# Performance work log

Hardware: AMD Instinct MI355X
Metric: run time of the kernel (lower is better)

Reference implementation:

```python
import jax, jax.numpy as jnp
import numpy as np

N_NODES = 100000
N_EDGES = 1600000
IN_F, HID_F, OUT_F = 256, 128, 32


def spmm(rows, cols, vals, x):
    # out[i] = sum_{e: rows[e]==i} vals[e] * x[cols[e]]  -- COO SpMM
    msgs = vals[:, None] * x[cols]            # [E, F] gathered weighted messages
    return jax.ops.segment_sum(msgs, rows, num_segments=N_NODES)


def setup_inputs() -> dict:
    key = jax.random.key(0)
    k = jax.random.split(key, 6)
    x = jax.random.normal(k[0], (N_NODES, IN_F), dtype=jnp.float32)
    adj_rows = jax.random.randint(k[1], (N_EDGES,), 0, N_NODES, dtype=jnp.int32)
    adj_cols = jax.random.randint(k[2], (N_EDGES,), 0, N_NODES, dtype=jnp.int32)
    adj_vals = jax.random.uniform(k[3], (N_EDGES,), dtype=jnp.float32)
    W1 = jax.random.normal(k[4], (IN_F, HID_F), dtype=jnp.float32) / np.sqrt(IN_F)
    W2 = jax.random.normal(k[5], (HID_F, OUT_F), dtype=jnp.float32) / np.sqrt(HID_F)
    return {"x": x, "adj_rows": adj_rows, "adj_cols": adj_cols,
            "adj_vals": adj_vals, "W1": W1, "W2": W2}


def reference(x, adj_rows, adj_cols, adj_vals, W1, W2):
    # TwoLayerGCN forward (eval mode: dropout = identity, labels=None)
    h = spmm(adj_rows, adj_cols, adj_vals, x @ W1)   # conv1: linear then A_hat @
    h = jax.nn.relu(h)
    out = spmm(adj_rows, adj_cols, adj_vals, h @ W2)  # conv2
    return out
```

## Files before the change

### kernel.cpp

```cpp
#include <hip/hip_runtime.h>
#include <hip/hip_bf16.h>

#define N_NODES 100000
#define IN_F 256
#define HID_F 128
#define OUT_F 32
#define NBUCK 391
#define BCAP  5120
#define ACHUNK 4096
#define NCHUNKS ((1600000 + ACHUNK - 1) / ACHUNK)

typedef __bf16 bf16x8 __attribute__((ext_vector_type(8)));
typedef __bf16 bf16x2 __attribute__((ext_vector_type(2)));
typedef float  f32x4  __attribute__((ext_vector_type(4)));

__global__ void cvt_w1t_kernel(const float* __restrict__ W1, __bf16* __restrict__ W1T) {
    int i = blockIdx.x * 256 + threadIdx.x;
    if (i >= IN_F * HID_F) return;
    int n = i >> 8, k = i & 255;
    W1T[i] = (__bf16)W1[k * HID_F + n];
}

__device__ __forceinline__
void bucketize_body(char* smem, int blk,
                    const int* __restrict__ rows, const int* __restrict__ cols,
                    const float* __restrict__ vals, int* __restrict__ gcnt,
                    int2* __restrict__ staged, int E) {
    int2* lcv  = (int2*)smem;
    int* lcnt  = (int*)(smem + ACHUNK * 8);
    int* loff  = lcnt + NBUCK;
    int* lcur  = loff + NBUCK;
    int* gbase = lcur + NBUCK;
    int* psum  = gbase + NBUCK;

    const int t    = threadIdx.x;
    const int base = blk * ACHUNK;

    for (int b = t; b < NBUCK; b += 256) lcnt[b] = 0;
    __syncthreads();

    int myrow[16];
#pragma unroll
    for (int i = 0; i < 16; ++i) {
        int e = base + t + i * 256;
        int r = (e < E) ? rows[e] : -1;
        myrow[i] = r;
        if (r >= 0) atomicAdd(&lcnt[r >> 8], 1);
    }
    __syncthreads();

    int s0 = (t * 2     < NBUCK) ? lcnt[t * 2]     : 0;
    int s1 = (t * 2 + 1 < NBUCK) ? lcnt[t * 2 + 1] : 0;
    int local = s0 + s1;
    psum[t] = local;
    __syncthreads();
    for (int off = 1; off < 256; off <<= 1) {
        int v = (t >= off) ? psum[t - off] : 0;
        __syncthreads();
        psum[t] += v;
        __syncthreads();
    }
    int excl = psum[t] - local;
    if (t * 2     < NBUCK) { loff[t * 2]     = excl;      lcur[t * 2]     = excl; }
    if (t * 2 + 1 < NBUCK) { loff[t * 2 + 1] = excl + s0; lcur[t * 2 + 1] = excl + s0; }
    __syncthreads();

#pragma unroll
    for (int i = 0; i < 16; ++i) {
        int r = myrow[i];
        if (r >= 0) {
            int e = base + t + i * 256;
            int posl = atomicAdd(&lcur[r >> 8], 1);
            lcv[posl] = make_int2(cols[e] | ((r & 255) << 20), __float_as_int(vals[e]));
        }
    }
    __syncthreads();

    for (int b = t; b < NBUCK; b += 256) {
        int c = lcnt[b];
        gbase[b] = c ? atomicAdd(&gcnt[b], c) : 0;
    }
    __syncthreads();

    int total = loff[NBUCK - 1] + lcnt[NBUCK - 1];
    for (int i = t; i < total; i += 256) {
        int lo = 0, hi = NBUCK - 1;
        while (lo < hi) {
            int mid = (lo + hi + 1) >> 1;
            if (loff[mid] <= i) lo = mid; else hi = mid - 1;
        }
        int idx = gbase[lo] + (i - loff[lo]);
        if (idx < BCAP)
            staged[(size_t)lo * BCAP + idx] = lcv[i];
    }
}

__device__ __forceinline__
void gemm1_body(char* smem, int blk,
                const float* __restrict__ x, const __bf16* __restrict__ W1T,
                __bf16* __restrict__ xw) {
    __bf16 (*Xs)[76] = (__bf16 (*)[76])smem;
    __bf16 (*Bs)[76] = (__bf16 (*)[76])(smem + 19456);

    const int r0   = blk * 128;
    const int t    = threadIdx.x;
    const int wv   = t >> 6;
    const int lane = t & 63;
    const int quad = lane >> 4;
    const int l15  = lane & 15;

    f32x4 acc[2][8];
#pragma unroll
    for (int rt = 0; rt < 2; ++rt)
#pragma unroll
        for (int nt = 0; nt < 8; ++nt)
            acc[rt][nt] = (f32x4){0.f, 0.f, 0.f, 0.f};

    const int srow = t >> 3;
    const int soct = t & 7;

    for (int q = 0; q < 4; ++q) {
        const int kq = q * 64;
#pragma unroll
        for (int j = 0; j < 4; ++j) {
            int row = j * 32 + srow;
            int gm = r0 + row;
            if (gm > N_NODES - 1) gm = N_NODES - 1;
            const float* xp = x + (size_t)gm * IN_F + kq + soct * 8;
            float4 f0 = *(const float4*)xp;
            float4 f1 = *(const float4*)(xp + 4);
            bf16x8 v = { (__bf16)f0.x, (__bf16)f0.y, (__bf16)f0.z, (__bf16)f0.w,
                         (__bf16)f1.x, (__bf16)f1.y, (__bf16)f1.z, (__bf16)f1.w };
            *(bf16x8*)(&Xs[row][soct * 8]) = v;
        }
#pragma unroll
        for (int i = 0; i < 4; ++i) {
            int idx = t + i * 256;
            int n = idx >> 3, kc = idx & 7;
            bf16x8 w = *(const bf16x8*)(W1T + n * 256 + kq + kc * 8);
            *(bf16x8*)(&Bs[n][kc * 8]) = w;
        }
        __syncthreads();

#pragma unroll
        for (int kt = 0; kt < 2; ++kt) {
            const int k0 = kt * 32;
            bf16x8 a[2];
#pragma unroll
            for (int rt = 0; rt < 2; ++rt)
                a[rt] = *(const bf16x8*)(&Xs[wv * 32 + rt * 16 + l15][k0 + quad * 8]);
            bf16x8 b[8];
#pragma unroll
            for (int nt = 0; nt < 8; ++nt)
                b[nt] = *(const bf16x8*)(&Bs[nt * 16 + l15][k0 + quad * 8]);
#pragma unroll
            for (int rt = 0; rt < 2; ++rt)
#pragma unroll
                for (int nt = 0; nt < 8; ++nt)
                    acc[rt][nt] = __builtin_amdgcn_mfma_f32_16x16x32_bf16(
                        a[rt], b[nt], acc[rt][nt], 0, 0, 0);
        }
        __syncthreads();
    }

#pragma unroll
    for (int rt = 0; rt < 2; ++rt)
#pragma unroll
        for (int nt = 0; nt < 8; ++nt)
#pragma unroll
            for (int reg = 0; reg < 4; ++reg) {
                int row = r0 + wv * 32 + rt * 16 + quad * 4 + reg;
                if (row < N_NODES)
                    xw[(size_t)row * HID_F + nt * 16 + l15] = (__bf16)acc[rt][nt][reg];
            }
}

__global__ __launch_bounds__(256, 4)
void fused_gemm1_bucketize_kernel(const float* __restrict__ x,
                                  const __bf16* __restrict__ W1T,
                                  __bf16* __restrict__ xw,
                                  const int* __restrict__ rows,
                                  const int* __restrict__ cols,
                                  const float* __restrict__ vals,
                                  int* __restrict__ gcnt,
                                  int2* __restrict__ staged, int E) {
    __shared__ __align__(16) char smem[40448];
    if (blockIdx.x < NCHUNKS)
        bucketize_body(smem, blockIdx.x, rows, cols, vals, gcnt, staged, E);
    else
        gemm1_body(smem, blockIdx.x - NCHUNKS, x, W1T, xw);
}

__global__ __launch_bounds__(256)
void bucket_csr_kernel(const int* __restrict__ gcnt,
                       const int2* __restrict__ staged,
                       int* __restrict__ row_ptr, int2* __restrict__ pedge) {
    __shared__ int2 lcv[BCAP];
    __shared__ int lcnt[256], loff[256], lcur[256];
    __shared__ int psum[256];
    __shared__ int boff[NBUCK + 1];

    const int b = blockIdx.x;
    const int t = threadIdx.x;

    int c0 = (t * 2     < NBUCK) ? min(gcnt[t * 2],     BCAP) : 0;
    int c1 = (t * 2 + 1 < NBUCK) ? min(gcnt[t * 2 + 1], BCAP) : 0;
    int local = c0 + c1;
    psum[t] = local;
    __syncthreads();
    for (int off = 1; off < 256; off <<= 1) {
        int v = (t >= off) ? psum[t - off] : 0;
        __syncthreads();
        psum[t] += v;
        __syncthreads();
    }
    int excl = psum[t] - local;
    if (t * 2     < NBUCK)  boff[t * 2]     = excl;
    if (t * 2 + 1 <= NBUCK) boff[t * 2 + 1] = excl + c0;
    __syncthreads();

    int n = gcnt[b]; if (n > BCAP) n = BCAP;
    const int2* sp = staged + (size_t)b * BCAP;
    const int base = boff[b];

    if (b == NBUCK - 1 && t == 0) row_ptr[N_NODES] = boff[NBUCK];

    lcnt[t] = 0;
    __syncthreads();
    for (int i = t; i < n; i += 256) {
        int2 v = sp[i];
        lcv[i] = v;
        atomicAdd(&lcnt[(v.x >> 20) & 255], 1);
    }
    __syncthreads();

    int v = lcnt[t];
    loff[t] = v;
    __syncthreads();
    for (int off = 1; off < 256; off <<= 1) {
        int u = (t >= off) ? loff[t - off] : 0;
        __syncthreads();
        loff[t] += u;
        __syncthreads();
    }
    int excl2 = loff[t] - v;
    lcur[t] = excl2;
    __syncthreads();

    int row = (b << 8) + t;
    if (row < N_NODES) row_ptr[row] = base + excl2;

    for (int i = t; i < n; i += 256) {
        int2 cv = lcv[i];
        int r = (cv.x >> 20) & 255;
        int pos = atomicAdd(&lcur[r], 1);
        pedge[base + pos] = make_int2(cv.x & 0xFFFFF, cv.y);
    }
}

__global__ __launch_bounds__(256)
void gemm2_mfma_kernel(const __bf16* __restrict__ h,
                       const float* __restrict__ W2,
                       __bf16* __restrict__ hw) {
    const int r0   = blockIdx.x * 128;
    const int wv   = threadIdx.x >> 6;
    const int lane = threadIdx.x & 63;
    const int quad = lane >> 4;
    const int l15  = lane & 15;

    __shared__ __bf16 W2T[32][136];

    for (int i = threadIdx.x; i < 32 * 128; i += 256) {
        int n = i & 31, k = i >> 5;
        W2T[n][k] = (__bf16)W2[k * OUT_F + n];
    }
    __syncthreads();

    f32x4 acc[2][2];
#pragma unroll
    for (int rt = 0; rt < 2; ++rt)
#pragma unroll
        for (int nt = 0; nt < 2; ++nt)
            acc[rt][nt] = (f32x4){0.f, 0.f, 0.f, 0.f};

#pragma unroll
    for (int kt = 0; kt < 4; ++kt) {
        const int k0 = kt * 32;
        bf16x8 a[2];
#pragma unroll
        for (int rt = 0; rt < 2; ++rt) {
            int gm = r0 + wv * 32 + rt * 16 + l15;
            if (gm > N_NODES - 1) gm = N_NODES - 1;
            a[rt] = *(const bf16x8*)(h + (size_t)gm * HID_F + k0 + quad * 8);
        }
        bf16x8 b[2];
#pragma unroll
        for (int nt = 0; nt < 2; ++nt)
            b[nt] = *(const bf16x8*)(&W2T[nt * 16 + l15][k0 + quad * 8]);
#pragma unroll
        for (int rt = 0; rt < 2; ++rt)
#pragma unroll
            for (int nt = 0; nt < 2; ++nt)
                acc[rt][nt] = __builtin_amdgcn_mfma_f32_16x16x32_bf16(
                    a[rt], b[nt], acc[rt][nt], 0, 0, 0);
    }

#pragma unroll
    for (int rt = 0; rt < 2; ++rt)
#pragma unroll
        for (int nt = 0; nt < 2; ++nt)
#pragma unroll
            for (int reg = 0; reg < 4; ++reg) {
                int row = r0 + wv * 32 + rt * 16 + quad * 4 + reg;
                if (row < N_NODES)
                    hw[(size_t)row * OUT_F + nt * 16 + l15] = (__bf16)acc[rt][nt][reg];
            }
}

__global__ __launch_bounds__(256)
void spmm1_kernel(const int* __restrict__ row_ptr,
                  const int2* __restrict__ pedge,
                  const __bf16* __restrict__ src,
                  __bf16* __restrict__ dst) {
    int row = __builtin_amdgcn_readfirstlane(blockIdx.x * 4 + (threadIdx.x >> 6));
    int lane = threadIdx.x & 63;
    if (row >= N_NODES) return;

    const int e0 = row_ptr[row];
    const int e1 = row_ptr[row + 1];

    float a0 = 0.f, a1 = 0.f;
    for (int e = e0; e < e1; e += 8) {
        int2 p[8];
#pragma unroll
        for (int j = 0; j < 8; ++j) {
            int ee = e + j;
            if (ee >= e1) ee = e1 - 1;
            p[j] = pedge[ee];
            if (e + j >= e1) p[j].y = 0;
        }
        bf16x2 s[8];
#pragma unroll
        for (int j = 0; j < 8; ++j)
            s[j] = ((const bf16x2*)(src + (size_t)p[j].x * HID_F))[lane];
#pragma unroll
        for (int j = 0; j < 8; ++j) {
            float v = __int_as_float(p[j].y);
            a0 += v * (float)s[j].x;
            a1 += v * (float)s[j].y;
        }
    }
    a0 = fmaxf(a0, 0.f);
    a1 = fmaxf(a1, 0.f);
    bf16x2 o = { (__bf16)a0, (__bf16)a1 };
    ((bf16x2*)(dst + (size_t)row * HID_F))[lane] = o;
}

__global__ __launch_bounds__(256)
void spmm2_kernel(const int* __restrict__ row_ptr,
                  const int2* __restrict__ pedge,
                  const __bf16* __restrict__ src,
                  float* __restrict__ dst) {
    long long gid = (long long)blockIdx.x * 256 + threadIdx.x;
    int row  = (int)(gid >> 4);
    int lane = (int)(gid & 15);
    if (row >= N_NODES) return;

    const int e0 = row_ptr[row];
    const int e1 = row_ptr[row + 1];

    float a0 = 0.f, a1 = 0.f;
    for (int e = e0; e < e1; e += 8) {
        int2 p[8];
#pragma unroll
        for (int j = 0; j < 8; ++j) {
            int ee = e + j;
            if (ee >= e1) ee = e1 - 1;
            p[j] = pedge[ee];
            if (e + j >= e1) p[j].y = 0;
        }
        bf16x2 s[8];
#pragma unroll
        for (int j = 0; j < 8; ++j)
            s[j] = ((const bf16x2*)(src + (size_t)p[j].x * OUT_F))[lane];
#pragma unroll
        for (int j = 0; j < 8; ++j) {
            float v = __int_as_float(p[j].y);
            a0 += v * (float)s[j].x;
            a1 += v * (float)s[j].y;
        }
    }
    ((float2*)(dst + (size_t)row * OUT_F))[lane] = make_float2(a0, a1);
}

extern "C" void kernel_launch(void* const* d_in, const int* in_sizes, int n_in,
                              void* d_out, int out_size, void* d_ws, size_t ws_size,
                              hipStream_t stream) {
    const float* x        = (const float*)d_in[0];
    const int*   adj_rows = (const int*)d_in[1];
    const int*   adj_cols = (const int*)d_in[2];
    const float* adj_vals = (const float*)d_in[3];
    const float* W1       = (const float*)d_in[4];
    const float* W2       = (const float*)d_in[5];
    float*       out      = (float*)d_out;
    const int E = in_sizes[1];

    char* p = (char*)d_ws;
    __bf16* W1T  = (__bf16*)p;  p += (size_t)IN_F * HID_F * sizeof(__bf16);
    __bf16* xw   = (__bf16*)p;  p += (size_t)N_NODES * HID_F * sizeof(__bf16);
    __bf16* h    = (__bf16*)p;  p += (size_t)N_NODES * HID_F * sizeof(__bf16);
    __bf16* hw   = (__bf16*)p;  p += (size_t)N_NODES * OUT_F * sizeof(__bf16);
    int*   row_ptr = (int*)p;   p += (size_t)(N_NODES + 1) * sizeof(int);
    int*   gcnt    = (int*)p;   p += ((NBUCK + 255) & ~255) * sizeof(int);
    p = (char*)(((uintptr_t)p + 15) & ~(uintptr_t)15);
    int2*  pedge   = (int2*)p;  p += (size_t)E * sizeof(int2);
    p = (char*)(((uintptr_t)p + 15) & ~(uintptr_t)15);
    int2*  staged  = (int2*)p;  p += (size_t)NBUCK * BCAP * sizeof(int2);

    hipMemsetAsync(gcnt, 0, (size_t)NBUCK * sizeof(int), stream);
    cvt_w1t_kernel<<<(IN_F * HID_F + 255) / 256, 256, 0, stream>>>(W1, W1T);

    fused_gemm1_bucketize_kernel<<<NCHUNKS + (N_NODES + 127) / 128, 256, 0, stream>>>(
        x, W1T, xw, adj_rows, adj_cols, adj_vals, gcnt, staged, E);

    bucket_csr_kernel<<<NBUCK, 256, 0, stream>>>(gcnt, staged, row_ptr, pedge);

    spmm1_kernel<<<(N_NODES + 3) / 4, 256, 0, stream>>>(row_ptr, pedge, xw, h);

    gemm2_mfma_kernel<<<(N_NODES + 127) / 128, 256, 0, stream>>>(h, W2, hw);
    {
        long long threads = (long long)N_NODES * 16;
        spmm2_kernel<<<(int)((threads + 255) / 256), 256, 0, stream>>>(
            row_ptr, pedge, hw, out);
    }
}
```

Measured before the change: 312.8 us.

## Fuse spmm1 with gemm2, swizzle gemm1 LDS and use direct global-to-LDS loads

Merges the first SpMM and the second dense GEMM into one kernel. Each wave aggregates a row into LDS, then multiplies it by W2 held in LDS, so the intermediate h never goes to global memory. The gemm1 path now pre-swizzles W1 into an XOR-swizzled layout that is loaded straight into LDS with global_load_lds. Its outputs are staged through LDS so global stores are coalesced. Bucketize chunk size drops to 3072 and occupancy is raised to 5 blocks per CU. The trade-offs are a per-block reload of W2 into LDS and a scalar dot product in place of MFMA for gemm2.

Result: slower. 400.7 us (+28.1%).

```diff
diff --git a/kernel.cpp b/kernel.cpp
--- a/kernel.cpp
+++ b/kernel.cpp
@@ -7,18 +7,31 @@
 #define OUT_F 32
 #define NBUCK 391
 #define BCAP  5120
-#define ACHUNK 4096
+#define ACHUNK 3072
+#define AITER (ACHUNK / 256)
 #define NCHUNKS ((1600000 + ACHUNK - 1) / ACHUNK)
+#define GEMM1_BLOCKS ((N_NODES + 127) / 128)
 
 typedef __bf16 bf16x8 __attribute__((ext_vector_type(8)));
 typedef __bf16 bf16x2 __attribute__((ext_vector_type(2)));
 typedef float  f32x4  __attribute__((ext_vector_type(4)));
 
-__global__ void cvt_w1t_kernel(const float* __restrict__ W1, __bf16* __restrict__ W1T) {
+__device__ __forceinline__ void gload_lds16(const void* g, void* l) {
+    __builtin_amdgcn_global_load_lds(
+        (const __attribute__((address_space(1))) unsigned int*)g,
+        (__attribute__((address_space(3))) unsigned int*)l, 16, 0, 0);
+}
+
+__global__ void cvt_w1s_kernel(const float* __restrict__ W1, __bf16* __restrict__ W1S) {
     int i = blockIdx.x * 256 + threadIdx.x;
     if (i >= IN_F * HID_F) return;
-    int n = i >> 8, k = i & 255;
-    W1T[i] = (__bf16)W1[k * HID_F + n];
+    int q  = i >> 13;
+    int pe = i & 8191;
+    int Pb = pe << 1;
+    int n  = Pb >> 7;
+    int Lb = Pb ^ ((n & 7) << 4);
+    int kq = (Lb & 127) >> 1;
+    W1S[i] = (__bf16)W1[(q * 64 + kq) * HID_F + n];
 }
 
 __device__ __forceinline__
@@ -39,9 +52,9 @@
     for (int b = t; b < NBUCK; b += 256) lcnt[b] = 0;
     __syncthreads();
 
-    int myrow[16];
-#pragma unroll
-    for (int i = 0; i < 16; ++i) {
+    int myrow[AITER];
+#pragma unroll
+    for (int i = 0; i < AITER; ++i) {
         int e = base + t + i * 256;
         int r = (e < E) ? rows[e] : -1;
         myrow[i] = r;
@@ -66,7 +79,7 @@
     __syncthreads();
 
 #pragma unroll
-    for (int i = 0; i < 16; ++i) {
+    for (int i = 0; i < AITER; ++i) {
         int r = myrow[i];
         if (r >= 0) {
             int e = base + t + i * 256;
@@ -97,10 +110,10 @@
 
 __device__ __forceinline__
 void gemm1_body(char* smem, int blk,
-                const float* __restrict__ x, const __bf16* __restrict__ W1T,
+                const float* __restrict__ x, const __bf16* __restrict__ W1S,
                 __bf16* __restrict__ xw) {
-    __bf16 (*Xs)[76] = (__bf16 (*)[76])smem;
-    __bf16 (*Bs)[76] = (__bf16 (*)[76])(smem + 19456);
+    char* Xs  = smem;
+    char* Bsm = smem + 16384;
 
     const int r0   = blk * 128;
     const int t    = threadIdx.x;
@@ -121,6 +134,11 @@
 
     for (int q = 0; q < 4; ++q) {
         const int kq = q * 64;
+#pragma unroll
+        for (int i2 = 0; i2 < 4; ++i2) {
+            int c = wv * 4 + i2;
+            gload_lds16(W1S + q * 8192 + c * 512 + lane * 8, Bsm + c * 1024);
+        }
 #pragma unroll
         for (int j = 0; j < 4; ++j) {
             int row = j * 32 + srow;
@@ -131,28 +149,26 @@
             float4 f1 = *(const float4*)(xp + 4);
             bf16x8 v = { (__bf16)f0.x, (__bf16)f0.y, (__bf16)f0.z, (__bf16)f0.w,
                          (__bf16)f1.x, (__bf16)f1.y, (__bf16)f1.z, (__bf16)f1.w };
-            *(bf16x8*)(&Xs[row][soct * 8]) = v;
-        }
-#pragma unroll
-        for (int i = 0; i < 4; ++i) {
-            int idx = t + i * 256;
-            int n = idx >> 3, kc = idx & 7;
-            bf16x8 w = *(const bf16x8*)(W1T + n * 256 + kq + kc * 8);
-            *(bf16x8*)(&Bs[n][kc * 8]) = w;
+            int byte = (row * 128 + soct * 16) ^ ((row & 7) << 4);
+            *(bf16x8*)(Xs + byte) = v;
         }
         __syncthreads();
 
 #pragma unroll
         for (int kt = 0; kt < 2; ++kt) {
-            const int k0 = kt * 32;
+            const int cb = (kt * 32 + quad * 8) * 2;
             bf16x8 a[2];
 #pragma unroll
-            for (int rt = 0; rt < 2; ++rt)
-                a[rt] = *(const bf16x8*)(&Xs[wv * 32 + rt * 16 + l15][k0 + quad * 8]);
+            for (int rt = 0; rt < 2; ++rt) {
+                int rA = wv * 32 + rt * 16 + l15;
+                a[rt] = *(const bf16x8*)(Xs + ((rA * 128 + cb) ^ ((rA & 7) << 4)));
+            }
             bf16x8 b[8];
 #pragma unroll
-            for (int nt = 0; nt < 8; ++nt)
-                b[nt] = *(const bf16x8*)(&Bs[nt * 16 + l15][k0 + quad * 8]);
+            for (int nt = 0; nt < 8; ++nt) {
+                int rB = nt * 16 + l15;
+                b[nt] = *(const bf16x8*)(Bsm + ((rB * 128 + cb) ^ ((rB & 7) << 4)));
+            }
 #pragma unroll
             for (int rt = 0; rt < 2; ++rt)
 #pragma unroll
@@ -163,32 +179,43 @@
         __syncthreads();
     }
 
+    __bf16 (*Ls)[128] = (__bf16 (*)[128])smem;
 #pragma unroll
     for (int rt = 0; rt < 2; ++rt)
 #pragma unroll
         for (int nt = 0; nt < 8; ++nt)
 #pragma unroll
-            for (int reg = 0; reg < 4; ++reg) {
-                int row = r0 + wv * 32 + rt * 16 + quad * 4 + reg;
-                if (row < N_NODES)
-                    xw[(size_t)row * HID_F + nt * 16 + l15] = (__bf16)acc[rt][nt][reg];
-            }
-}
-
-__global__ __launch_bounds__(256, 4)
+            for (int reg = 0; reg < 4; ++reg)
+                Ls[wv * 32 + rt * 16 + quad * 4 + reg][nt * 16 + l15] =
+                    (__bf16)acc[rt][nt][reg];
+    __syncthreads();
+
+#pragma unroll
+    for (int i = 0; i < 8; ++i) {
+        int id = i * 256 + t;
+        int row = id >> 4, cc = id & 15;
+        int g = r0 + row;
+        if (g < N_NODES) {
+            bf16x8 v = *(const bf16x8*)(&Ls[row][cc * 8]);
+            *(bf16x8*)(xw + (size_t)g * HID_F + cc * 8) = v;
+        }
+    }
+}
+
+__global__ __launch_bounds__(256, 5)
 void fused_gemm1_bucketize_kernel(const float* __restrict__ x,
-                                  const __bf16* __restrict__ W1T,
+                                  const __bf16* __restrict__ W1S,
                                   __bf16* __restrict__ xw,
                                   const int* __restrict__ rows,
                                   const int* __restrict__ cols,
                                   const float* __restrict__ vals,
                                   int* __restrict__ gcnt,
                                   int2* __restrict__ staged, int E) {
-    __shared__ __align__(16) char smem[40448];
+    __shared__ __align__(16) char smem[32768];
     if (blockIdx.x < NCHUNKS)
         bucketize_body(smem, blockIdx.x, rows, cols, vals, gcnt, staged, E);
     else
-        gemm1_body(smem, blockIdx.x - NCHUNKS, x, W1T, xw);
+        gemm1_body(smem, blockIdx.x - NCHUNKS, x, W1S, xw);
 }
 
 __global__ __launch_bounds__(256)
@@ -259,72 +286,25 @@
 }
 
 __global__ __launch_bounds__(256)
-void gemm2_mfma_kernel(const __bf16* __restrict__ h,
-                       const float* __restrict__ W2,
-                       __bf16* __restrict__ hw) {
-    const int r0   = blockIdx.x * 128;
-    const int wv   = threadIdx.x >> 6;
-    const int lane = threadIdx.x & 63;
-    const int quad = lane >> 4;
-    const int l15  = lane & 15;
-
+void spmm1_gemm2_kernel(const int* __restrict__ row_ptr,
+                        const int2* __restrict__ pedge,
+                        const __bf16* __restrict__ src,
+                        const float* __restrict__ W2,
+                        __bf16* __restrict__ hw) {
     __shared__ __bf16 W2T[32][136];
-
-    for (int i = threadIdx.x; i < 32 * 128; i += 256) {
+    __shared__ __align__(16) bf16x2 hs[4][64];
+
+    const int t    = threadIdx.x;
+    const int wv   = t >> 6;
+    const int lane = t & 63;
+
+    for (int i = t; i < 32 * 128; i += 256) {
         int n = i & 31, k = i >> 5;
         W2T[n][k] = (__bf16)W2[k * OUT_F + n];
     }
     __syncthreads();
 
-    f32x4 acc[2][2];
-#pragma unroll
-    for (int rt = 0; rt < 2; ++rt)
-#pragma unroll
-        for (int nt = 0; nt < 2; ++nt)
-            acc[rt][nt] = (f32x4){0.f, 0.f, 0.f, 0.f};
-
-#pragma unroll
-    for (int kt = 0; kt < 4; ++kt) {
-        const int k0 = kt * 32;
-        bf16x8 a[2];
-#pragma unroll
-        for (int rt = 0; rt < 2; ++rt) {
-            int gm = r0 + wv * 32 + rt * 16 + l15;
-            if (gm > N_NODES - 1) gm = N_NODES - 1;
-            a[rt] = *(const bf16x8*)(h + (size_t)gm * HID_F + k0 + quad * 8);
-        }
-        bf16x8 b[2];
-#pragma unroll
-        for (int nt = 0; nt < 2; ++nt)
-            b[nt] = *(const bf16x8*)(&W2T[nt * 16 + l15][k0 + quad * 8]);
-#pragma unroll
-        for (int rt = 0; rt < 2; ++rt)
-#pragma unroll
-            for (int nt = 0; nt < 2; ++nt)
-                acc[rt][nt] = __builtin_amdgcn_mfma_f32_16x16x32_bf16(
-                    a[rt], b[nt], acc[rt][nt], 0, 0, 0);
-    }
-
-#pragma unroll
-    for (int rt = 0; rt < 2; ++rt)
-#pragma unroll
-        for (int nt = 0; nt < 2; ++nt)
-#pragma unroll
-            for (int reg = 0; reg < 4; ++reg) {
-                int row = r0 + wv * 32 + rt * 16 + quad * 4 + reg;
-                if (row < N_NODES)
-                    hw[(size_t)row * OUT_F + nt * 16 + l15] = (__bf16)acc[rt][nt][reg];
-            }
-}
-
-__global__ __launch_bounds__(256)
-void spmm1_kernel(const int* __restrict__ row_ptr,
-                  const int2* __restrict__ pedge,
-                  const __bf16* __restrict__ src,
-                  __bf16* __restrict__ dst) {
-    int row = __builtin_amdgcn_readfirstlane(blockIdx.x * 4 + (threadIdx.x >> 6));
-    int lane = threadIdx.x & 63;
-    if (row >= N_NODES) return;
+    int row = __builtin_amdgcn_readfirstlane(blockIdx.x * 4 + wv);
 
     const int e0 = row_ptr[row];
     const int e1 = row_ptr[row + 1];
@@ -352,8 +332,25 @@
     }
     a0 = fmaxf(a0, 0.f);
     a1 = fmaxf(a1, 0.f);
-    bf16x2 o = { (__bf16)a0, (__bf16)a1 };
-    ((bf16x2*)(dst + (size_t)row * HID_F))[lane] = o;
+    hs[wv][lane] = (bf16x2){ (__bf16)a0, (__bf16)a1 };
+    __syncthreads();
+
+    const int o     = lane & 31;
+    const int halfk = lane >> 5;
+    const __bf16* hr = (const __bf16*)&hs[wv][0];
+    float s = 0.f;
+#pragma unroll
+    for (int kk = 0; kk < 64; kk += 8) {
+        int k = halfk * 64 + kk;
+        bf16x8 hv  = *(const bf16x8*)(hr + k);
+        bf16x8 wv8 = *(const bf16x8*)(&W2T[o][k]);
+#pragma unroll
+        for (int j = 0; j < 8; ++j)
+            s += (float)hv[j] * (float)wv8[j];
+    }
+    s += __shfl_xor(s, 32);
+    if (halfk == 0)
+        hw[(size_t)row * OUT_F + o] = (__bf16)s;
 }
 
 __global__ __launch_bounds__(256)
@@ -406,9 +403,8 @@
     const int E = in_sizes[1];
 
     char* p = (char*)d_ws;
-    __bf16* W1T  = (__bf16*)p;  p += (size_t)IN_F * HID_F * sizeof(__bf16);
+    __bf16* W1S  = (__bf16*)p;  p += (size_t)IN_F * HID_F * sizeof(__bf16);
     __bf16* xw   = (__bf16*)p;  p += (size_t)N_NODES * HID_F * sizeof(__bf16);
-    __bf16* h    = (__bf16*)p;  p += (size_t)N_NODES * HID_F * sizeof(__bf16);
     __bf16* hw   = (__bf16*)p;  p += (size_t)N_NODES * OUT_F * sizeof(__bf16);
     int*   row_ptr = (int*)p;   p += (size_t)(N_NODES + 1) * sizeof(int);
     int*   gcnt    = (int*)p;   p += ((NBUCK + 255) & ~255) * sizeof(int);
@@ -418,16 +414,15 @@
     int2*  staged  = (int2*)p;  p += (size_t)NBUCK * BCAP * sizeof(int2);
 
     hipMemsetAsync(gcnt, 0, (size_t)NBUCK * sizeof(int), stream);
-    cvt_w1t_kernel<<<(IN_F * HID_F + 255) / 256, 256, 0, stream>>>(W1, W1T);
-
-    fused_gemm1_bucketize_kernel<<<NCHUNKS + (N_NODES + 127) / 128, 256, 0, stream>>>(
-        x, W1T, xw, adj_rows, adj_cols, adj_vals, gcnt, staged, E);
+    cvt_w1s_kernel<<<(IN_F * HID_F + 255) / 256, 256, 0, stream>>>(W1, W1S);
+
+    fused_gemm1_bucketize_kernel<<<NCHUNKS + GEMM1_BLOCKS, 256, 0, stream>>>(
+        x, W1S, xw, adj_rows, adj_cols, adj_vals, gcnt, staged, E);
 
     bucket_csr_kernel<<<NBUCK, 256, 0, stream>>>(gcnt, staged, row_ptr, pedge);
 
-    spmm1_kernel<<<(N_NODES + 3) / 4, 256, 0, stream>>>(row_ptr, pedge, xw, h);
-
-    gemm2_mfma_kernel<<<(N_NODES + 127) / 128, 256, 0, stream>>>(h, W2, hw);
+    spmm1_gemm2_kernel<<<N_NODES / 4, 256, 0, stream>>>(row_ptr, pedge, xw, W2, hw);
+
     {
         long long threads = (long long)N_NODES * 16;
         spmm2_kernel<<<(int)((threads + 255) / 256), 256, 0, stream>>>(
```
